# Kernel optimization log

Hardware: AMD Instinct MI355X
Metric: run time of the kernel (lower is better)

The kernel has to match this reference:

```python
import jax, jax.numpy as jnp
import numpy as np

EPS = 1e-6
B, N, K = 4, 65536, 16
D_IN, D_OUT, DH = 8, 16, 8  # DH = d_out // 2


def _bn(x, g, b):
    # train-mode BatchNorm2d over (B, N, K) per channel (channels-last here)
    m = jnp.mean(x, axis=(0, 1, 2))
    v = jnp.var(x, axis=(0, 1, 2))
    return (x - m) * jax.lax.rsqrt(v + EPS) * g + b


def _conv(x, w, b):
    # 1x1 Conv2d == per-point linear; x: (B,N,K,Cin), w: (Cout,Cin)
    return jnp.einsum('bnki,oi->bnko', x, w) + b


def _lse(coords, feats, idx, w, b, g, bt):
    # coords: (B,N,3), feats: (B,N,1,D), idx: (B,N,K)
    nbrs = jnp.take_along_axis(coords[:, :, None, :], idx[:, :, :, None], axis=1)  # (B,N,K,3)
    ctr = jnp.broadcast_to(coords[:, :, None, :], nbrs.shape)
    dist = jnp.ones(idx.shape + (1,), dtype=coords.dtype)  # torch path passes idx only -> dist = ones
    enc = jnp.concatenate([ctr, nbrs, ctr - nbrs, dist], axis=-1)  # (B,N,K,10)
    h = jax.nn.relu(_bn(_conv(enc, w, b), g, bt))
    f = jnp.broadcast_to(feats, idx.shape + (feats.shape[-1],))
    return jnp.concatenate([h, f], axis=-1)  # (B,N,K,2*D)


def _pool(x, sw, w, b, g, bt):
    # attentive pooling: softmax over neighbor axis K (axis=2)
    scores = jax.nn.softmax(jnp.einsum('bnki,oi->bnko', x, sw), axis=2)
    agg = jnp.sum(scores * x, axis=2, keepdims=True)  # (B,N,1,C)
    return jax.nn.relu(_bn(_conv(agg, w, b), g, bt))


def setup_inputs() -> dict:
    key = jax.random.key(0)
    ks = jax.random.split(key, 16)
    rn = lambda k, s: (0.1 * jax.random.normal(k, s)).astype(jnp.float32)
    inp = {
        'coords': jax.random.normal(ks[0], (B, N, 3), dtype=jnp.float32),
        'features': jax.random.normal(ks[1], (B, D_IN, N, 1), dtype=jnp.float32),
        'idx': jax.random.randint(ks[2], (B, N, K), 0, N, dtype=jnp.int32),
        # mlp1: d_in -> d_out//2, no bn, LeakyReLU(0.2)
        'w1': rn(ks[3], (DH, D_IN)), 'b1': jnp.zeros((DH,), jnp.float32),
        # lse1 mlp: 10 -> d_out//2, bn + ReLU
        'lse1_w': rn(ks[4], (DH, 10)), 'lse1_b': jnp.zeros((DH,), jnp.float32),
        'lse1_g': jnp.ones((DH,), jnp.float32), 'lse1_bt': jnp.zeros((DH,), jnp.float32),
        # pool1: in d_out -> out d_out//2
        'p1_sw': rn(ks[5], (D_OUT, D_OUT)),
        'p1_w': rn(ks[6], (DH, D_OUT)), 'p1_b': jnp.zeros((DH,), jnp.float32),
        'p1_g': jnp.ones((DH,), jnp.float32), 'p1_bt': jnp.zeros((DH,), jnp.float32),
        # lse2
        'lse2_w': rn(ks[7], (DH, 10)), 'lse2_b': jnp.zeros((DH,), jnp.float32),
        'lse2_g': jnp.ones((DH,), jnp.float32), 'lse2_bt': jnp.zeros((DH,), jnp.float32),
        # pool2: in d_out -> out d_out
        'p2_sw': rn(ks[8], (D_OUT, D_OUT)),
        'p2_w': rn(ks[9], (D_OUT, D_OUT)), 'p2_b': jnp.zeros((D_OUT,), jnp.float32),
        'p2_g': jnp.ones((D_OUT,), jnp.float32), 'p2_bt': jnp.zeros((D_OUT,), jnp.float32),
        # mlp2: d_out -> 2*d_out (no bn/act)
        'w2': rn(ks[10], (2 * D_OUT, D_OUT)), 'b2': jnp.zeros((2 * D_OUT,), jnp.float32),
        # shortcut: d_in -> 2*d_out, bn, no act
        'sc_w': rn(ks[11], (2 * D_OUT, D_IN)), 'sc_b': jnp.zeros((2 * D_OUT,), jnp.float32),
        'sc_g': jnp.ones((2 * D_OUT,), jnp.float32), 'sc_bt': jnp.zeros((2 * D_OUT,), jnp.float32),
    }
    return inp


def reference(coords, features, idx, w1, b1, lse1_w, lse1_b, lse1_g, lse1_bt,
              p1_sw, p1_w, p1_b, p1_g, p1_bt, lse2_w, lse2_b, lse2_g, lse2_bt,
              p2_sw, p2_w, p2_b, p2_g, p2_bt, w2, b2, sc_w, sc_b, sc_g, sc_bt):
    feats = jnp.transpose(features, (0, 2, 3, 1))  # (B,N,1,d_in) channels-last
    x = jax.nn.leaky_relu(_conv(feats, w1, b1), 0.2)           # (B,N,1,DH)
    x = _lse(coords, x, idx, lse1_w, lse1_b, lse1_g, lse1_bt)  # (B,N,K,D_OUT)
    x = _pool(x, p1_sw, p1_w, p1_b, p1_g, p1_bt)               # (B,N,1,DH)
    x = _lse(coords, x, idx, lse2_w, lse2_b, lse2_g, lse2_bt)  # (B,N,K,D_OUT)
    x = _pool(x, p2_sw, p2_w, p2_b, p2_g, p2_bt)               # (B,N,1,D_OUT)
    out = jax.nn.leaky_relu(
        _conv(x, w2, b2) + _bn(_conv(feats, sc_w, sc_b), sc_g, sc_bt), 0.01)
    return jnp.transpose(out, (0, 3, 1, 2))  # (B, 2*d_out, N, 1)
```

## Files before the change

### kernel.cpp

```cpp
#include <hip/hip_runtime.h>

#define NB 4
#define NN 65536
#define NK 16
#define NP (NB * NN)
#define BN_EPS 1e-6f

#define WS_ENC_M   0
#define WS_SC_M    32
#define WS_S_Y2    96
#define WS_SS_Y2   104
#define WS_S_Y4    112
#define WS_SS_Y4   128
#define WS_Y2      1024
#define WS_Y4      (1024 + NP * 8)

template <int NCH>
__device__ inline void blockReduceAtomic(float (&v)[NCH], float* __restrict__ dst) {
    __shared__ float red[4][NCH];
    const int lane = threadIdx.x & 63;
    const int wv = threadIdx.x >> 6;
    __syncthreads();
#pragma unroll
    for (int c = 0; c < NCH; c++) {
        float x = v[c];
#pragma unroll
        for (int off = 32; off > 0; off >>= 1) x += __shfl_xor(x, off, 64);
        if (lane == 0) red[wv][c] = x;
    }
    __syncthreads();
    for (int c = threadIdx.x; c < NCH; c += 256)
        atomicAdd(dst + c, red[0][c] + red[1][c] + red[2][c] + red[3][c]);
    __syncthreads();
}

__device__ inline void bn_from_enc(const float* __restrict__ M, const float* __restrict__ w,
                                   float b, float g, float bt, float& sc, float& sh) {
    float u[6];
    u[0] = w[0] + w[6]; u[1] = w[1] + w[7]; u[2] = w[2] + w[8];
    u[3] = w[3] - w[6]; u[4] = w[4] - w[7]; u[5] = w[5] - w[8];
    const float beta = b + w[9];
    float lin = 0.f;
#pragma unroll
    for (int i = 0; i < 6; i++) lin += u[i] * M[i];
    float quad = u[0] * u[0] * M[6] + 2.f * u[0] * u[1] * M[7] + 2.f * u[0] * u[2] * M[8]
               + u[1] * u[1] * M[9] + 2.f * u[1] * u[2] * M[10] + u[2] * u[2] * M[11];
#pragma unroll
    for (int i = 0; i < 3; i++)
#pragma unroll
        for (int j = 0; j < 3; j++) quad += 2.f * u[i] * u[3 + j] * M[12 + i * 3 + j];
    quad += u[3] * u[3] * M[21] + 2.f * u[3] * u[4] * M[22] + 2.f * u[3] * u[5] * M[23]
          + u[4] * u[4] * M[24] + 2.f * u[4] * u[5] * M[25] + u[5] * u[5] * M[26];
    const float cnt = (float)NP * (float)NK;
    const float sum = lin + cnt * beta;
    const float ss = quad + 2.f * beta * lin + cnt * beta * beta;
    const float m = sum / cnt, v = ss / cnt - m * m;
    sc = g * rsqrtf(v + BN_EPS);
    sh = bt - m * sc;
}

__global__ __launch_bounds__(256) void k_stats(
    const float* __restrict__ coords, const float* __restrict__ feats,
    const int* __restrict__ idx, float* __restrict__ ws) {
    const int tid = threadIdx.x;
    const int p = blockIdx.x * 256 + tid;
    const int b = p >> 16;
    const int n = p & (NN - 1);

    {
        float accf[44];
        float f[8];
#pragma unroll
        for (int i = 0; i < 8; i++) f[i] = feats[(b * 8 + i) * NN + n];
#pragma unroll
        for (int i = 0; i < 8; i++) accf[i] = f[i];
        int t2 = 8;
#pragma unroll
        for (int i = 0; i < 8; i++)
#pragma unroll
            for (int j = i; j < 8; j++) accf[t2++] = f[i] * f[j];
        blockReduceAtomic<44>(accf, ws + WS_SC_M);
    }

    const float cx = coords[3 * p], cy = coords[3 * p + 1], cz = coords[3 * p + 2];
    const float* cb = coords + b * NN * 3;
    const int4* ip = (const int4*)idx + p * 4;
    float sn0 = 0.f, sn1 = 0.f, sn2 = 0.f;
    float m00 = 0.f, m01 = 0.f, m02 = 0.f, m11 = 0.f, m12 = 0.f, m22 = 0.f;
#pragma unroll
    for (int q = 0; q < 4; q++) {
        int4 v = ip[q];
        int jj[4] = {v.x, v.y, v.z, v.w};
#pragma unroll
        for (int e = 0; e < 4; e++) {
            const int j = jj[e];
            const float nx = cb[3 * j], ny = cb[3 * j + 1], nz = cb[3 * j + 2];
            sn0 += nx; sn1 += ny; sn2 += nz;
            m00 += nx * nx; m01 += nx * ny; m02 += nx * nz;
            m11 += ny * ny; m12 += ny * nz; m22 += nz * nz;
        }
    }
    float acc[27];
    acc[0] = 16.f * cx; acc[1] = 16.f * cy; acc[2] = 16.f * cz;
    acc[3] = sn0; acc[4] = sn1; acc[5] = sn2;
    acc[6] = 16.f * cx * cx; acc[7] = 16.f * cx * cy; acc[8] = 16.f * cx * cz;
    acc[9] = 16.f * cy * cy; acc[10] = 16.f * cy * cz; acc[11] = 16.f * cz * cz;
    acc[12] = cx * sn0; acc[13] = cx * sn1; acc[14] = cx * sn2;
    acc[15] = cy * sn0; acc[16] = cy * sn1; acc[17] = cy * sn2;
    acc[18] = cz * sn0; acc[19] = cz * sn1; acc[20] = cz * sn2;
    acc[21] = m00; acc[22] = m01; acc[23] = m02;
    acc[24] = m11; acc[25] = m12; acc[26] = m22;
    blockReduceAtomic<27>(acc, ws + WS_ENC_M);
}

__global__ __launch_bounds__(256) void k_pool1(
    const float* __restrict__ coords, const float* __restrict__ feats,
    const int* __restrict__ idx,
    const float* __restrict__ w1, const float* __restrict__ b1,
    const float* __restrict__ lse1_w, const float* __restrict__ lse1_b,
    const float* __restrict__ lse1_g, const float* __restrict__ lse1_bt,
    const float* __restrict__ p1_sw, const float* __restrict__ p1_w,
    const float* __restrict__ p1_b, float* __restrict__ ws) {
    __shared__ float an[24], dc3[24], dcon[8], sws[64], pws[128], pbs[8], w1s[64], b1s[8];
    const int tid = threadIdx.x;
    if (tid < 8) {
        const int c = tid;
        const float* w = lse1_w + c * 10;
        float sc, sh;
        bn_from_enc(ws + WS_ENC_M, w, lse1_b[c], lse1_g[c], lse1_bt[c], sc, sh);
#pragma unroll
        for (int i = 0; i < 3; i++) {
            an[c * 3 + i] = sc * (w[3 + i] - w[6 + i]);
            dc3[c * 3 + i] = sc * (w[i] + w[6 + i]);
        }
        dcon[c] = sc * (lse1_b[c] + w[9]) + sh;
        b1s[c] = b1[c]; pbs[c] = p1_b[c];
    }
    if (tid < 64) {
        w1s[tid] = w1[tid];
        sws[tid] = p1_sw[(tid >> 3) * 16 + (tid & 7)];
    }
    if (tid < 128) pws[tid] = p1_w[tid];
    __syncthreads();

    const int p = blockIdx.x * 256 + tid;
    const int b = p >> 16;
    const int n = p & (NN - 1);
    const float cx = coords[3 * p], cy = coords[3 * p + 1], cz = coords[3 * p + 2];
    const float* cb = coords + b * NN * 3;
    float d[8];
#pragma unroll
    for (int c = 0; c < 8; c++)
        d[c] = dc3[c * 3] * cx + dc3[c * 3 + 1] * cy + dc3[c * 3 + 2] * cz + dcon[c];
    const int4* ip = (const int4*)idx + p * 4;
    float l[8] = {}, ac[8] = {};
#pragma unroll
    for (int q = 0; q < 4; q++) {
        int4 v = ip[q];
        int jj[4] = {v.x, v.y, v.z, v.w};
#pragma unroll
        for (int e = 0; e < 4; e++) {
            const int j = jj[e];
            const float nx = cb[3 * j], ny = cb[3 * j + 1], nz = cb[3 * j + 2];
            float h[8];
#pragma unroll
            for (int c = 0; c < 8; c++) {
                float y = an[c * 3] * nx + an[c * 3 + 1] * ny + an[c * 3 + 2] * nz + d[c];
                h[c] = y > 0.f ? y : 0.f;
            }
#pragma unroll
            for (int o = 0; o < 8; o++) {
                float s = 0.f;
#pragma unroll
                for (int i = 0; i < 8; i++) s += h[i] * sws[o * 8 + i];
                float e2 = __expf(s);
                l[o] += e2; ac[o] += e2 * h[o];
            }
        }
    }
    float f[8];
#pragma unroll
    for (int i = 0; i < 8; i++) f[i] = feats[(b * 8 + i) * NN + n];
    float agg[16];
#pragma unroll
    for (int o = 0; o < 8; o++) agg[o] = ac[o] / l[o];
#pragma unroll
    for (int jq = 0; jq < 8; jq++) {
        float y = b1s[jq];
#pragma unroll
        for (int i = 0; i < 8; i++) y += f[i] * w1s[jq * 8 + i];
        agg[8 + jq] = y > 0.f ? y : 0.2f * y;
    }
    float st[16];
#pragma unroll
    for (int c = 0; c < 8; c++) {
        float y = pbs[c];
#pragma unroll
        for (int o = 0; o < 16; o++) y += agg[o] * pws[c * 16 + o];
        ws[WS_Y2 + c * NP + p] = y;
        st[c] = y; st[8 + c] = y * y;
    }
    blockReduceAtomic<16>(st, ws + WS_S_Y2);
}

__global__ __launch_bounds__(256) void k_pool2(
    const float* __restrict__ coords, const int* __restrict__ idx,
    const float* __restrict__ lse2_w, const float* __restrict__ lse2_b,
    const float* __restrict__ lse2_g, const float* __restrict__ lse2_bt,
    const float* __restrict__ p1_g, const float* __restrict__ p1_bt,
    const float* __restrict__ p2_sw, const float* __restrict__ p2_w,
    const float* __restrict__ p2_b, float* __restrict__ ws) {
    __shared__ float an[24], dc3[24], dcon[8], p1sc[8], p1sh[8],
        sws[64], pws[256], pbs[16];
    const int tid = threadIdx.x;
    if (tid < 8) {
        const int c = tid;
        const float* w = lse2_w + c * 10;
        float sc, sh;
        bn_from_enc(ws + WS_ENC_M, w, lse2_b[c], lse2_g[c], lse2_bt[c], sc, sh);
#pragma unroll
        for (int i = 0; i < 3; i++) {
            an[c * 3 + i] = sc * (w[3 + i] - w[6 + i]);
            dc3[c * 3 + i] = sc * (w[i] + w[6 + i]);
        }
        dcon[c] = sc * (lse2_b[c] + w[9]) + sh;
    } else if (tid < 16) {
        const int c = tid - 8;
        const float cP = 1.f / (float)NP;
        float m = ws[WS_S_Y2 + c] * cP, v = ws[WS_SS_Y2 + c] * cP - m * m;
        float sc = p1_g[c] * rsqrtf(v + BN_EPS);
        p1sc[c] = sc; p1sh[c] = p1_bt[c] - m * sc;
    }
    if (tid < 64) sws[tid] = p2_sw[(tid >> 3) * 16 + (tid & 7)];
    if (tid < 256) pws[tid] = p2_w[tid];
    if (tid < 16) pbs[tid] = p2_b[tid];
    __syncthreads();

    const int p = blockIdx.x * 256 + tid;
    const int b = p >> 16;
    const float cx = coords[3 * p], cy = coords[3 * p + 1], cz = coords[3 * p + 2];
    const float* cb = coords + b * NN * 3;
    float d[8];
#pragma unroll
    for (int c = 0; c < 8; c++)
        d[c] = dc3[c * 3] * cx + dc3[c * 3 + 1] * cy + dc3[c * 3 + 2] * cz + dcon[c];
    const int4* ip = (const int4*)idx + p * 4;
    float l[8] = {}, ac[8] = {};
#pragma unroll
    for (int q = 0; q < 4; q++) {
        int4 v = ip[q];
        int jj[4] = {v.x, v.y, v.z, v.w};
#pragma unroll
        for (int e = 0; e < 4; e++) {
            const int j = jj[e];
            const float nx = cb[3 * j], ny = cb[3 * j + 1], nz = cb[3 * j + 2];
            float h[8];
#pragma unroll
            for (int c = 0; c < 8; c++) {
                float y = an[c * 3] * nx + an[c * 3 + 1] * ny + an[c * 3 + 2] * nz + d[c];
                h[c] = y > 0.f ? y : 0.f;
            }
#pragma unroll
            for (int o = 0; o < 8; o++) {
                float s = 0.f;
#pragma unroll
                for (int i = 0; i < 8; i++) s += h[i] * sws[o * 8 + i];
                float e2 = __expf(s);
                l[o] += e2; ac[o] += e2 * h[o];
            }
        }
    }
    float agg[16];
#pragma unroll
    for (int o = 0; o < 8; o++) agg[o] = ac[o] / l[o];
#pragma unroll
    for (int c = 0; c < 8; c++) {
        float y = ws[WS_Y2 + c * NP + p] * p1sc[c] + p1sh[c];
        agg[8 + c] = y > 0.f ? y : 0.f;
    }
    float st[32];
#pragma unroll
    for (int c = 0; c < 16; c++) {
        float y = pbs[c];
#pragma unroll
        for (int o = 0; o < 16; o++) y += agg[o] * pws[c * 16 + o];
        ws[WS_Y4 + c * NP + p] = y;
        st[c] = y; st[16 + c] = y * y;
    }
    blockReduceAtomic<32>(st, ws + WS_S_Y4);
}

__global__ __launch_bounds__(256) void k_final(
    const float* __restrict__ feats, const float* __restrict__ w2,
    const float* __restrict__ b2, const float* __restrict__ sc_w,
    const float* __restrict__ sc_b, const float* __restrict__ p2_g,
    const float* __restrict__ p2_bt, const float* __restrict__ sc_g,
    const float* __restrict__ sc_bt, const float* __restrict__ ws,
    float* __restrict__ out) {
    __shared__ float w2s[512], b2s[32], scws[256], scbs[32],
        p2sc[16], p2sh[16], scsc[32], scsh[32];
    const int tid = threadIdx.x;
    for (int i = tid; i < 512; i += 256) w2s[i] = w2[i];
    if (tid < 256) scws[tid] = sc_w[tid];
    if (tid < 32) {
        b2s[tid] = b2[tid]; scbs[tid] = sc_b[tid];
        const int c = tid;
        const float* w = sc_w + c * 8;
        const float* S = ws + WS_SC_M;
        float lin = 0.f;
#pragma unroll
        for (int i = 0; i < 8; i++) lin += w[i] * S[i];
        float quad = 0.f;
        int t2 = 0;
#pragma unroll
        for (int i = 0; i < 8; i++)
#pragma unroll
            for (int j = i; j < 8; j++) {
                const float mm = S[8 + t2++];
                quad += (i == j ? 1.f : 2.f) * w[i] * w[j] * mm;
            }
        const float cnt = (float)NP;
        const float bb = sc_b[c];
        const float sum = lin + cnt * bb;
        const float ss = quad + 2.f * bb * lin + cnt * bb * bb;
        const float m = sum / cnt, v = ss / cnt - m * m;
        const float sc = sc_g[c] * rsqrtf(v + BN_EPS);
        scsc[c] = sc; scsh[c] = sc_bt[c] - m * sc;
    }
    if (tid < 16) {
        const int c = tid;
        const float cP = 1.f / (float)NP;
        float m = ws[WS_S_Y4 + c] * cP, v = ws[WS_SS_Y4 + c] * cP - m * m;
        float sc = p2_g[c] * rsqrtf(v + BN_EPS);
        p2sc[c] = sc; p2sh[c] = p2_bt[c] - m * sc;
    }
    __syncthreads();

    const int p = blockIdx.x * 256 + tid;
    const int b = p >> 16;
    const int n = p & (NN - 1);
    float x4[16];
#pragma unroll
    for (int c = 0; c < 16; c++) {
        float y = ws[WS_Y4 + c * NP + p] * p2sc[c] + p2sh[c];
        x4[c] = y > 0.f ? y : 0.f;
    }
    float f[8];
#pragma unroll
    for (int i = 0; i < 8; i++) f[i] = feats[(b * 8 + i) * NN + n];
#pragma unroll
    for (int c = 0; c < 32; c++) {
        float s = scbs[c];
#pragma unroll
        for (int i = 0; i < 8; i++) s += f[i] * scws[c * 8 + i];
        s = s * scsc[c] + scsh[c];
        float m = b2s[c];
#pragma unroll
        for (int o = 0; o < 16; o++) m += x4[o] * w2s[c * 16 + o];
        float v = m + s;
        out[(b * 32 + c) * NN + n] = v > 0.f ? v : 0.01f * v;
    }
}

extern "C" void kernel_launch(void* const* d_in, const int* in_sizes, int n_in,
                              void* d_out, int out_size, void* d_ws, size_t ws_size,
                              hipStream_t stream) {
    (void)in_sizes; (void)n_in; (void)out_size; (void)ws_size;
    const float* coords = (const float*)d_in[0];
    const float* features = (const float*)d_in[1];
    const int* idx = (const int*)d_in[2];
    const float* w1 = (const float*)d_in[3];
    const float* b1 = (const float*)d_in[4];
    const float* lse1_w = (const float*)d_in[5];
    const float* lse1_b = (const float*)d_in[6];
    const float* lse1_g = (const float*)d_in[7];
    const float* lse1_bt = (const float*)d_in[8];
    const float* p1_sw = (const float*)d_in[9];
    const float* p1_w = (const float*)d_in[10];
    const float* p1_b = (const float*)d_in[11];
    const float* p1_g = (const float*)d_in[12];
    const float* p1_bt = (const float*)d_in[13];
    const float* lse2_w = (const float*)d_in[14];
    const float* lse2_b = (const float*)d_in[15];
    const float* lse2_g = (const float*)d_in[16];
    const float* lse2_bt = (const float*)d_in[17];
    const float* p2_sw = (const float*)d_in[18];
    const float* p2_w = (const float*)d_in[19];
    const float* p2_b = (const float*)d_in[20];
    const float* p2_g = (const float*)d_in[21];
    const float* p2_bt = (const float*)d_in[22];
    const float* w2 = (const float*)d_in[23];
    const float* b2 = (const float*)d_in[24];
    const float* sc_w = (const float*)d_in[25];
    const float* sc_b = (const float*)d_in[26];
    const float* sc_g = (const float*)d_in[27];
    const float* sc_bt = (const float*)d_in[28];
    float* ws = (float*)d_ws;
    float* out = (float*)d_out;

    const int NBLK = NP / 256;
    hipMemsetAsync(ws, 0, 144 * sizeof(float), stream);
    k_stats<<<NBLK, 256, 0, stream>>>(coords, features, idx, ws);
    k_pool1<<<NBLK, 256, 0, stream>>>(coords, features, idx, w1, b1, lse1_w, lse1_b,
                                      lse1_g, lse1_bt, p1_sw, p1_w, p1_b, ws);
    k_pool2<<<NBLK, 256, 0, stream>>>(coords, idx, lse2_w, lse2_b, lse2_g, lse2_bt,
                                      p1_g, p1_bt, p2_sw, p2_w, p2_b, ws);
    k_final<<<NBLK, 256, 0, stream>>>(features, w2, b2, sc_w, sc_b, p2_g, p2_bt,
                                      sc_g, sc_bt, ws, out);
}
```

Baseline: 349.1 us.

## Split neighbor work across threads and move feature stats into pool1

The pool kernels now assign four threads per point, each handling four neighbors, and combine the softmax partial sums with cross-lane shuffles. k_stats uses two threads per point and no longer computes the shortcut feature moments, which are accumulated in k_pool1 through shared memory instead. Block reductions use shuffle-based partial sums, exp is computed as exp2 with log2e folded into the weights, and division is replaced by a hardware reciprocal. More threads and more outstanding gathers should hide the random coordinate gather latency better, at the cost of duplicated per-point center work and extra shuffles.

```diff
diff --git a/kernel.cpp b/kernel.cpp
--- a/kernel.cpp
+++ b/kernel.cpp
@@ -5,6 +5,7 @@
 #define NK 16
 #define NP (NB * NN)
 #define BN_EPS 1e-6f
+#define LOG2E 1.44269504088896f
 
 #define WS_ENC_M   0
 #define WS_SC_M    32
@@ -60,56 +61,37 @@
 }
 
 __global__ __launch_bounds__(256) void k_stats(
-    const float* __restrict__ coords, const float* __restrict__ feats,
-    const int* __restrict__ idx, float* __restrict__ ws) {
-    const int tid = threadIdx.x;
-    const int p = blockIdx.x * 256 + tid;
+    const float* __restrict__ coords, const int* __restrict__ idx,
+    float* __restrict__ ws) {
+    const int t = blockIdx.x * 256 + threadIdx.x;
+    const int p = t >> 1;
     const int b = p >> 16;
-    const int n = p & (NN - 1);
-
-    {
-        float accf[44];
-        float f[8];
-#pragma unroll
-        for (int i = 0; i < 8; i++) f[i] = feats[(b * 8 + i) * NN + n];
-#pragma unroll
-        for (int i = 0; i < 8; i++) accf[i] = f[i];
-        int t2 = 8;
-#pragma unroll
-        for (int i = 0; i < 8; i++)
-#pragma unroll
-            for (int j = i; j < 8; j++) accf[t2++] = f[i] * f[j];
-        blockReduceAtomic<44>(accf, ws + WS_SC_M);
-    }
-
     const float cx = coords[3 * p], cy = coords[3 * p + 1], cz = coords[3 * p + 2];
     const float* cb = coords + b * NN * 3;
-    const int4* ip = (const int4*)idx + p * 4;
-    float sn0 = 0.f, sn1 = 0.f, sn2 = 0.f;
-    float m00 = 0.f, m01 = 0.f, m02 = 0.f, m11 = 0.f, m12 = 0.f, m22 = 0.f;
-#pragma unroll
-    for (int q = 0; q < 4; q++) {
+    const int4* ip = (const int4*)idx + t * 2;
+    float acc[27] = {};
+#pragma unroll
+    for (int q = 0; q < 2; q++) {
         int4 v = ip[q];
         int jj[4] = {v.x, v.y, v.z, v.w};
+        float nx[4], ny[4], nz[4];
 #pragma unroll
         for (int e = 0; e < 4; e++) {
-            const int j = jj[e];
-            const float nx = cb[3 * j], ny = cb[3 * j + 1], nz = cb[3 * j + 2];
-            sn0 += nx; sn1 += ny; sn2 += nz;
-            m00 += nx * nx; m01 += nx * ny; m02 += nx * nz;
-            m11 += ny * ny; m12 += ny * nz; m22 += nz * nz;
-        }
-    }
-    float acc[27];
-    acc[0] = 16.f * cx; acc[1] = 16.f * cy; acc[2] = 16.f * cz;
-    acc[3] = sn0; acc[4] = sn1; acc[5] = sn2;
-    acc[6] = 16.f * cx * cx; acc[7] = 16.f * cx * cy; acc[8] = 16.f * cx * cz;
-    acc[9] = 16.f * cy * cy; acc[10] = 16.f * cy * cz; acc[11] = 16.f * cz * cz;
-    acc[12] = cx * sn0; acc[13] = cx * sn1; acc[14] = cx * sn2;
-    acc[15] = cy * sn0; acc[16] = cy * sn1; acc[17] = cy * sn2;
-    acc[18] = cz * sn0; acc[19] = cz * sn1; acc[20] = cz * sn2;
-    acc[21] = m00; acc[22] = m01; acc[23] = m02;
-    acc[24] = m11; acc[25] = m12; acc[26] = m22;
+            nx[e] = cb[3 * jj[e]]; ny[e] = cb[3 * jj[e] + 1]; nz[e] = cb[3 * jj[e] + 2];
+        }
+#pragma unroll
+        for (int e = 0; e < 4; e++) {
+            acc[3] += nx[e]; acc[4] += ny[e]; acc[5] += nz[e];
+            acc[12] += cx * nx[e]; acc[13] += cx * ny[e]; acc[14] += cx * nz[e];
+            acc[15] += cy * nx[e]; acc[16] += cy * ny[e]; acc[17] += cy * nz[e];
+            acc[18] += cz * nx[e]; acc[19] += cz * ny[e]; acc[20] += cz * nz[e];
+            acc[21] += nx[e] * nx[e]; acc[22] += nx[e] * ny[e]; acc[23] += nx[e] * nz[e];
+            acc[24] += ny[e] * ny[e]; acc[25] += ny[e] * nz[e]; acc[26] += nz[e] * nz[e];
+        }
+    }
+    acc[0] = 8.f * cx; acc[1] = 8.f * cy; acc[2] = 8.f * cz;
+    acc[6] = 8.f * cx * cx; acc[7] = 8.f * cx * cy; acc[8] = 8.f * cx * cz;
+    acc[9] = 8.f * cy * cy; acc[10] = 8.f * cy * cz; acc[11] = 8.f * cz * cz;
     blockReduceAtomic<27>(acc, ws + WS_ENC_M);
 }
 
@@ -122,6 +104,8 @@
     const float* __restrict__ p1_sw, const float* __restrict__ p1_w,
     const float* __restrict__ p1_b, float* __restrict__ ws) {
     __shared__ float an[24], dc3[24], dcon[8], sws[64], pws[128], pbs[8], w1s[64], b1s[8];
+    __shared__ float red[4][16];
+    __shared__ float scst[64 * 44];
     const int tid = threadIdx.x;
     if (tid < 8) {
         const int c = tid;
@@ -138,12 +122,14 @@
     }
     if (tid < 64) {
         w1s[tid] = w1[tid];
-        sws[tid] = p1_sw[(tid >> 3) * 16 + (tid & 7)];
+        sws[tid] = p1_sw[(tid >> 3) * 16 + (tid & 7)] * LOG2E;
     }
     if (tid < 128) pws[tid] = p1_w[tid];
     __syncthreads();
 
-    const int p = blockIdx.x * 256 + tid;
+    const int g = tid >> 2;
+    const int q = tid & 3;
+    const int p = blockIdx.x * 64 + g;
     const int b = p >> 16;
     const int n = p & (NN - 1);
     const float cx = coords[3 * p], cy = coords[3 * p + 1], cz = coords[3 * p + 2];
@@ -152,55 +138,87 @@
 #pragma unroll
     for (int c = 0; c < 8; c++)
         d[c] = dc3[c * 3] * cx + dc3[c * 3 + 1] * cy + dc3[c * 3 + 2] * cz + dcon[c];
-    const int4* ip = (const int4*)idx + p * 4;
+    const int4 v = ((const int4*)idx)[blockIdx.x * 256 + tid];
+    int jj[4] = {v.x, v.y, v.z, v.w};
+    float nx[4], ny[4], nz[4];
+#pragma unroll
+    for (int e = 0; e < 4; e++) {
+        nx[e] = cb[3 * jj[e]]; ny[e] = cb[3 * jj[e] + 1]; nz[e] = cb[3 * jj[e] + 2];
+    }
     float l[8] = {}, ac[8] = {};
 #pragma unroll
-    for (int q = 0; q < 4; q++) {
-        int4 v = ip[q];
-        int jj[4] = {v.x, v.y, v.z, v.w};
-#pragma unroll
-        for (int e = 0; e < 4; e++) {
-            const int j = jj[e];
-            const float nx = cb[3 * j], ny = cb[3 * j + 1], nz = cb[3 * j + 2];
-            float h[8];
-#pragma unroll
-            for (int c = 0; c < 8; c++) {
-                float y = an[c * 3] * nx + an[c * 3 + 1] * ny + an[c * 3 + 2] * nz + d[c];
-                h[c] = y > 0.f ? y : 0.f;
-            }
-#pragma unroll
-            for (int o = 0; o < 8; o++) {
-                float s = 0.f;
-#pragma unroll
-                for (int i = 0; i < 8; i++) s += h[i] * sws[o * 8 + i];
-                float e2 = __expf(s);
-                l[o] += e2; ac[o] += e2 * h[o];
-            }
-        }
-    }
+    for (int e = 0; e < 4; e++) {
+        float h[8];
+#pragma unroll
+        for (int c = 0; c < 8; c++) {
+            float y = an[c * 3] * nx[e] + an[c * 3 + 1] * ny[e] + an[c * 3 + 2] * nz[e] + d[c];
+            h[c] = y > 0.f ? y : 0.f;
+        }
+#pragma unroll
+        for (int o = 0; o < 8; o++) {
+            float s = 0.f;
+#pragma unroll
+            for (int i = 0; i < 8; i++) s += h[i] * sws[o * 8 + i];
+            float e2 = exp2f(s);
+            l[o] += e2; ac[o] += e2 * h[o];
+        }
+    }
+#pragma unroll
+    for (int o = 0; o < 8; o++) {
+        l[o] += __shfl_xor(l[o], 1, 64);  l[o] += __shfl_xor(l[o], 2, 64);
+        ac[o] += __shfl_xor(ac[o], 1, 64); ac[o] += __shfl_xor(ac[o], 2, 64);
+    }
+    float agg[16];
+#pragma unroll
+    for (int o = 0; o < 8; o++) agg[o] = ac[o] * __builtin_amdgcn_rcpf(l[o]);
     float f[8];
 #pragma unroll
     for (int i = 0; i < 8; i++) f[i] = feats[(b * 8 + i) * NN + n];
-    float agg[16];
-#pragma unroll
-    for (int o = 0; o < 8; o++) agg[o] = ac[o] / l[o];
-#pragma unroll
-    for (int jq = 0; jq < 8; jq++) {
-        float y = b1s[jq];
-#pragma unroll
-        for (int i = 0; i < 8; i++) y += f[i] * w1s[jq * 8 + i];
-        agg[8 + jq] = y > 0.f ? y : 0.2f * y;
-    }
-    float st[16];
-#pragma unroll
-    for (int c = 0; c < 8; c++) {
+#pragma unroll
+    for (int j = 0; j < 8; j++) {
+        float y = b1s[j];
+#pragma unroll
+        for (int i = 0; i < 8; i++) y += f[i] * w1s[j * 8 + i];
+        agg[8 + j] = y > 0.f ? y : 0.2f * y;
+    }
+    float sy[2], syy[2];
+#pragma unroll
+    for (int t = 0; t < 2; t++) {
+        const int c = 2 * q + t;
         float y = pbs[c];
 #pragma unroll
         for (int o = 0; o < 16; o++) y += agg[o] * pws[c * 16 + o];
         ws[WS_Y2 + c * NP + p] = y;
-        st[c] = y; st[8 + c] = y * y;
-    }
-    blockReduceAtomic<16>(st, ws + WS_S_Y2);
+        sy[t] = y; syy[t] = y * y;
+    }
+#pragma unroll
+    for (int off = 4; off < 64; off <<= 1) {
+        sy[0] += __shfl_xor(sy[0], off, 64);  sy[1] += __shfl_xor(sy[1], off, 64);
+        syy[0] += __shfl_xor(syy[0], off, 64); syy[1] += __shfl_xor(syy[1], off, 64);
+    }
+    if (q == 0) {
+        float* s0 = scst + g * 44;
+#pragma unroll
+        for (int i = 0; i < 8; i++) s0[i] = f[i];
+        int t2 = 8;
+#pragma unroll
+        for (int i = 0; i < 8; i++)
+#pragma unroll
+            for (int j2 = i; j2 < 8; j2++) s0[t2++] = f[i] * f[j2];
+    }
+    const int lane = tid & 63, wv = tid >> 6;
+    if (lane < 4) {
+        red[wv][2 * lane] = sy[0]; red[wv][2 * lane + 1] = sy[1];
+        red[wv][8 + 2 * lane] = syy[0]; red[wv][8 + 2 * lane + 1] = syy[1];
+    }
+    __syncthreads();
+    if (tid < 16)
+        atomicAdd(ws + WS_S_Y2 + tid, red[0][tid] + red[1][tid] + red[2][tid] + red[3][tid]);
+    if (tid < 44) {
+        float s2 = 0.f;
+        for (int g2 = 0; g2 < 64; g2++) s2 += scst[g2 * 44 + tid];
+        atomicAdd(ws + WS_SC_M + tid, s2);
+    }
 }
 
 __global__ __launch_bounds__(256) void k_pool2(
@@ -210,8 +228,8 @@
     const float* __restrict__ p1_g, const float* __restrict__ p1_bt,
     const float* __restrict__ p2_sw, const float* __restrict__ p2_w,
     const float* __restrict__ p2_b, float* __restrict__ ws) {
-    __shared__ float an[24], dc3[24], dcon[8], p1sc[8], p1sh[8],
-        sws[64], pws[256], pbs[16];
+    __shared__ float an[24], dc3[24], dcon[8], p1sc[8], p1sh[8], sws[64], pws[256], pbs[16];
+    __shared__ float red[4][32];
     const int tid = threadIdx.x;
     if (tid < 8) {
         const int c = tid;
@@ -227,16 +245,18 @@
     } else if (tid < 16) {
         const int c = tid - 8;
         const float cP = 1.f / (float)NP;
-        float m = ws[WS_S_Y2 + c] * cP, v = ws[WS_SS_Y2 + c] * cP - m * m;
-        float sc = p1_g[c] * rsqrtf(v + BN_EPS);
+        float m = ws[WS_S_Y2 + c] * cP, vv = ws[WS_SS_Y2 + c] * cP - m * m;
+        float sc = p1_g[c] * rsqrtf(vv + BN_EPS);
         p1sc[c] = sc; p1sh[c] = p1_bt[c] - m * sc;
     }
-    if (tid < 64) sws[tid] = p2_sw[(tid >> 3) * 16 + (tid & 7)];
+    if (tid < 64) sws[tid] = p2_sw[(tid >> 3) * 16 + (tid & 7)] * LOG2E;
     if (tid < 256) pws[tid] = p2_w[tid];
     if (tid < 16) pbs[tid] = p2_b[tid];
     __syncthreads();
 
-    const int p = blockIdx.x * 256 + tid;
+    const int g = tid >> 2;
+    const int q = tid & 3;
+    const int p = blockIdx.x * 64 + g;
     const int b = p >> 16;
     const float cx = coords[3 * p], cy = coords[3 * p + 1], cz = coords[3 * p + 2];
     const float* cb = coords + b * NN * 3;
@@ -244,50 +264,73 @@
 #pragma unroll
     for (int c = 0; c < 8; c++)
         d[c] = dc3[c * 3] * cx + dc3[c * 3 + 1] * cy + dc3[c * 3 + 2] * cz + dcon[c];
-    const int4* ip = (const int4*)idx + p * 4;
+    const int4 v = ((const int4*)idx)[blockIdx.x * 256 + tid];
+    int jj[4] = {v.x, v.y, v.z, v.w};
+    float nx[4], ny[4], nz[4];
+#pragma unroll
+    for (int e = 0; e < 4; e++) {
+        nx[e] = cb[3 * jj[e]]; ny[e] = cb[3 * jj[e] + 1]; nz[e] = cb[3 * jj[e] + 2];
+    }
     float l[8] = {}, ac[8] = {};
 #pragma unroll
-    for (int q = 0; q < 4; q++) {
-        int4 v = ip[q];
-        int jj[4] = {v.x, v.y, v.z, v.w};
-#pragma unroll
-        for (int e = 0; e < 4; e++) {
-            const int j = jj[e];
-            const float nx = cb[3 * j], ny = cb[3 * j + 1], nz = cb[3 * j + 2];
-            float h[8];
-#pragma unroll
-            for (int c = 0; c < 8; c++) {
-                float y = an[c * 3] * nx + an[c * 3 + 1] * ny + an[c * 3 + 2] * nz + d[c];
-                h[c] = y > 0.f ? y : 0.f;
-            }
-#pragma unroll
-            for (int o = 0; o < 8; o++) {
-                float s = 0.f;
-#pragma unroll
-                for (int i = 0; i < 8; i++) s += h[i] * sws[o * 8 + i];
-                float e2 = __expf(s);
-                l[o] += e2; ac[o] += e2 * h[o];
-            }
-        }
+    for (int e = 0; e < 4; e++) {
+        float h[8];
+#pragma unroll
+        for (int c = 0; c < 8; c++) {
+            float y = an[c * 3] * nx[e] + an[c * 3 + 1] * ny[e] + an[c * 3 + 2] * nz[e] + d[c];
+            h[c] = y > 0.f ? y : 0.f;
+        }
+#pragma unroll
+        for (int o = 0; o < 8; o++) {
+            float s = 0.f;
+#pragma unroll
+            for (int i = 0; i < 8; i++) s += h[i] * sws[o * 8 + i];
+            float e2 = exp2f(s);
+            l[o] += e2; ac[o] += e2 * h[o];
+        }
+    }
+#pragma unroll
+    for (int o = 0; o < 8; o++) {
+        l[o] += __shfl_xor(l[o], 1, 64);  l[o] += __shfl_xor(l[o], 2, 64);
+        ac[o] += __shfl_xor(ac[o], 1, 64); ac[o] += __shfl_xor(ac[o], 2, 64);
     }
     float agg[16];
 #pragma unroll
-    for (int o = 0; o < 8; o++) agg[o] = ac[o] / l[o];
+    for (int o = 0; o < 8; o++) agg[o] = ac[o] * __builtin_amdgcn_rcpf(l[o]);
 #pragma unroll
     for (int c = 0; c < 8; c++) {
         float y = ws[WS_Y2 + c * NP + p] * p1sc[c] + p1sh[c];
         agg[8 + c] = y > 0.f ? y : 0.f;
     }
-    float st[32];
-#pragma unroll
-    for (int c = 0; c < 16; c++) {
+    float sy[4], syy[4];
+#pragma unroll
+    for (int t = 0; t < 4; t++) {
+        const int c = 4 * q + t;
         float y = pbs[c];
 #pragma unroll
         for (int o = 0; o < 16; o++) y += agg[o] * pws[c * 16 + o];
         ws[WS_Y4 + c * NP + p] = y;
-        st[c] = y; st[16 + c] = y * y;
-    }
-    blockReduceAtomic<32>(st, ws + WS_S_Y4);
+        sy[t] = y; syy[t] = y * y;
+    }
+#pragma unroll
+    for (int off = 4; off < 64; off <<= 1) {
+#pragma unroll
+        for (int t = 0; t < 4; t++) {
+            sy[t] += __shfl_xor(sy[t], off, 64);
+            syy[t] += __shfl_xor(syy[t], off, 64);
+        }
+    }
+    const int lane = tid & 63, wv = tid >> 6;
+    if (lane < 4) {
+#pragma unroll
+        for (int t = 0; t < 4; t++) {
+            red[wv][4 * lane + t] = sy[t];
+            red[wv][16 + 4 * lane + t] = syy[t];
+        }
+    }
+    __syncthreads();
+    if (tid < 32)
+        atomicAdd(ws + WS_S_Y4 + tid, red[0][tid] + red[1][tid] + red[2][tid] + red[3][tid]);
 }
 
 __global__ __launch_bounds__(256) void k_final(
@@ -323,15 +366,15 @@
         const float bb = sc_b[c];
         const float sum = lin + cnt * bb;
         const float ss = quad + 2.f * bb * lin + cnt * bb * bb;
-        const float m = sum / cnt, v = ss / cnt - m * m;
-        const float sc = sc_g[c] * rsqrtf(v + BN_EPS);
+        const float m = sum / cnt, vv = ss / cnt - m * m;
+        const float sc = sc_g[c] * rsqrtf(vv + BN_EPS);
         scsc[c] = sc; scsh[c] = sc_bt[c] - m * sc;
     }
     if (tid < 16) {
         const int c = tid;
         const float cP = 1.f / (float)NP;
-        float m = ws[WS_S_Y4 + c] * cP, v = ws[WS_SS_Y4 + c] * cP - m * m;
-        float sc = p2_g[c] * rsqrtf(v + BN_EPS);
+        float m = ws[WS_S_Y4 + c] * cP, vv = ws[WS_SS_Y4 + c] * cP - m * m;
+        float sc = p2_g[c] * rsqrtf(vv + BN_EPS);
         p2sc[c] = sc; p2sh[c] = p2_bt[c] - m * sc;
     }
     __syncthreads();
@@ -357,8 +400,8 @@
         float m = b2s[c];
 #pragma unroll
         for (int o = 0; o < 16; o++) m += x4[o] * w2s[c * 16 + o];
-        float v = m + s;
-        out[(b * 32 + c) * NN + n] = v > 0.f ? v : 0.01f * v;
+        float vv = m + s;
+        out[(b * 32 + c) * NN + n] = vv > 0.f ? vv : 0.01f * vv;
     }
 }
 
@@ -398,13 +441,12 @@
     float* ws = (float*)d_ws;
     float* out = (float*)d_out;
 
-    const int NBLK = NP / 256;
     hipMemsetAsync(ws, 0, 144 * sizeof(float), stream);
-    k_stats<<<NBLK, 256, 0, stream>>>(coords, features, idx, ws);
-    k_pool1<<<NBLK, 256, 0, stream>>>(coords, features, idx, w1, b1, lse1_w, lse1_b,
-                                      lse1_g, lse1_bt, p1_sw, p1_w, p1_b, ws);
-    k_pool2<<<NBLK, 256, 0, stream>>>(coords, idx, lse2_w, lse2_b, lse2_g, lse2_bt,
-                                      p1_g, p1_bt, p2_sw, p2_w, p2_b, ws);
-    k_final<<<NBLK, 256, 0, stream>>>(features, w2, b2, sc_w, sc_b, p2_g, p2_bt,
-                                      sc_g, sc_bt, ws, out);
-}
+    k_stats<<<NP * 2 / 256, 256, 0, stream>>>(coords, idx, ws);
+    k_pool1<<<NP / 64, 256, 0, stream>>>(coords, features, idx, w1, b1, lse1_w, lse1_b,
+                                         lse1_g, lse1_bt, p1_sw, p1_w, p1_b, ws);
+    k_pool2<<<NP / 64, 256, 0, stream>>>(coords, idx, lse2_w, lse2_b, lse2_g, lse2_bt,
+                                         p1_g, p1_bt, p2_sw, p2_w, p2_b, ws);
+    k_final<<<NP / 256, 256, 0, stream>>>(features, w2, b2, sc_w, sc_b, p2_g, p2_bt,
+                                          sc_g, sc_bt, ws, out);
+}
```

Result: slower. 397.7 us (+13.9%).
